# Optimization experiments

Hardware: AMD Instinct MI355X
Metric: run time of the kernel (lower is better)

## Reference

```python
import jax, jax.numpy as jnp
import numpy as np

B, H, N, D = 4, 16, 2048, 64


def setup_inputs() -> dict:
    key = jax.random.key(0)
    kq, kk, kv, km, kb = jax.random.split(key, 5)
    q = jax.random.normal(kq, (B, H, N, D), dtype=jnp.float32)
    k = jax.random.normal(kk, (B, H, N, D), dtype=jnp.float32)
    v = jax.random.normal(kv, (B, H, N, D), dtype=jnp.float32)
    # mostly-True mask so no row is fully masked
    mask = jax.random.uniform(km, (B, 1, N, N)) > 0.1
    attn_bias = jax.random.normal(kb, (1, H, N, N), dtype=jnp.float32)
    return {"q": q, "k": k, "v": v, "mask": mask, "attn_bias": attn_bias}


def reference(q, k, v, mask, attn_bias):
    scale = q.shape[-1] ** -0.5
    # sim: [B,H,N,N]
    sim = jnp.einsum('bhid,bhjd->bhij', q, k) * scale
    sim = sim + attn_bias
    neg = -jnp.finfo(sim.dtype).max
    sim = jnp.where(mask, sim, neg)
    attn = jax.nn.softmax(sim, axis=-1)
    out = jnp.einsum('bhij,bhjd->bhid', attn, v)
    return out
```

## Files before the change

### kernel.cpp

```cpp
#include <hip/hip_runtime.h>
#include <hip/hip_bf16.h>

typedef __bf16 bf16_t;
typedef bf16_t bf16x8 __attribute__((ext_vector_type(8)));
typedef float  floatx4 __attribute__((ext_vector_type(4)));

constexpr int Bb = 4, Hh = 16, Nn = 2048, Dd = 64;
constexpr int BM = 64;
constexpr int BN = 64;
constexpr int WM = 16;
constexpr float SCALE = 0.125f;
constexpr float NEG   = -3.4028234663852886e38f;

__global__ __launch_bounds__(256, 4)
void attn_fwd(const float* __restrict__ qg,
              const float* __restrict__ kg,
              const float* __restrict__ vg,
              const void*  __restrict__ maskg,
              const float* __restrict__ biasg,
              float* __restrict__ outg)
{
    __shared__ bf16x8 k_lds[512];
    __shared__ bf16x8 v_lds[512];
    __shared__ bf16x8 p_lds[4][128];

    const int tid  = threadIdx.x;
    const int wave = tid >> 6;
    const int lane = tid & 63;
    const int ln   = lane & 15;
    const int lq   = lane >> 4;

    const int id = blockIdx.x;
    const int b  = id & 3;
    const int h  = (id >> 2) & 15;
    const int mt = id >> 6;

    const int probe = ((const int*)maskg)[lane];
    const bool mask_i32 = __all(probe == 0 || probe == 1);
    const int*           mi = (const int*)maskg;
    const unsigned char* mb = (const unsigned char*)maskg;

    const size_t head  = (size_t)(b*Hh + h) * Nn * Dd;
    const int    qbase = mt*BM + wave*WM;

    bf16x8 qa[2];
    {
        const float* qp = qg + head + (size_t)(qbase + ln)*Dd + lq*8;
        #pragma unroll
        for (int kk = 0; kk < 2; ++kk) {
            float4 f0 = *(const float4*)(qp + kk*32);
            float4 f1 = *(const float4*)(qp + kk*32 + 4);
            bf16x8 a;
            a[0]=(bf16_t)f0.x; a[1]=(bf16_t)f0.y; a[2]=(bf16_t)f0.z; a[3]=(bf16_t)f0.w;
            a[4]=(bf16_t)f1.x; a[5]=(bf16_t)f1.y; a[6]=(bf16_t)f1.z; a[7]=(bf16_t)f1.w;
            qa[kk] = a;
        }
    }

    floatx4 o_acc[4];
    #pragma unroll
    for (int i = 0; i < 4; ++i) o_acc[i] = (floatx4){0.f,0.f,0.f,0.f};
    float mx[4], lsum[4];
    #pragma unroll
    for (int r = 0; r < 4; ++r) { mx[r] = -__builtin_inff(); lsum[r] = 0.f; }

    const int skey = tid >> 2;
    const int sd0  = (tid & 3) * 16;
    const int sblk = skey >> 4, sn = skey & 15;
    const int vkk  = skey >> 5, vq = (skey >> 3) & 3, vj = skey & 7;
    bf16_t* vl = (bf16_t*)v_lds;
    bf16_t* pl = (bf16_t*)p_lds[wave];

    for (int kt = 0; kt < Nn/BN; ++kt) {
        __syncthreads();
        {
            const float* kp = kg + head + (size_t)(kt*BN + skey)*Dd + sd0;
            const float* vp = vg + head + (size_t)(kt*BN + skey)*Dd + sd0;
            float kvv[16], vvv[16];
            *(float4*)(kvv+ 0) = *(const float4*)(kp+ 0);
            *(float4*)(kvv+ 4) = *(const float4*)(kp+ 4);
            *(float4*)(kvv+ 8) = *(const float4*)(kp+ 8);
            *(float4*)(kvv+12) = *(const float4*)(kp+12);
            *(float4*)(vvv+ 0) = *(const float4*)(vp+ 0);
            *(float4*)(vvv+ 4) = *(const float4*)(vp+ 4);
            *(float4*)(vvv+ 8) = *(const float4*)(vp+ 8);
            *(float4*)(vvv+12) = *(const float4*)(vp+12);
            #pragma unroll
            for (int g = 0; g < 2; ++g) {
                const int dg = sd0 + g*8;
                const int kkg = dg >> 5, qg2 = (dg >> 3) & 3;
                bf16x8 c;
                #pragma unroll
                for (int j = 0; j < 8; ++j) c[j] = (bf16_t)kvv[g*8+j];
                k_lds[(sblk*2 + kkg)*64 + qg2*16 + sn] = c;
            }
            #pragma unroll
            for (int t = 0; t < 16; ++t) {
                const int d = sd0 + t;
                const int nb = d >> 4, nn2 = d & 15;
                vl[(((vkk*4 + nb)*64 + vq*16 + nn2) << 3) | vj] = (bf16_t)vvv[t];
            }
        }
        __syncthreads();

        floatx4 s_acc[4];
        #pragma unroll
        for (int i = 0; i < 4; ++i) s_acc[i] = (floatx4){0.f,0.f,0.f,0.f};
        #pragma unroll
        for (int blk = 0; blk < 4; ++blk)
            #pragma unroll
            for (int kk = 0; kk < 2; ++kk)
                s_acc[blk] = __builtin_amdgcn_mfma_f32_16x16x32_bf16(
                    qa[kk], k_lds[(blk*2+kk)*64 + lane], s_acc[blk], 0, 0, 0);

        float sv[4][4], rmax[4];
        const size_t col0 = (size_t)kt*BN + ln;
        #pragma unroll
        for (int r = 0; r < 4; ++r) {
            const int m = qbase + lq*4 + r;
            const size_t brow = ((size_t)h*Nn + m)*Nn + col0;
            const size_t mrow = ((size_t)b*Nn + m)*Nn + col0;
            rmax[r] = NEG;
            #pragma unroll
            for (int blk = 0; blk < 4; ++blk) {
                float val = s_acc[blk][r]*SCALE + biasg[brow + blk*16];
                const bool ok = mask_i32 ? (mi[mrow + blk*16] != 0)
                                         : (mb[mrow + blk*16] != 0);
                val = ok ? val : NEG;
                sv[r][blk] = val;
                rmax[r] = fmaxf(rmax[r], val);
            }
        }
        #pragma unroll
        for (int off = 1; off < 16; off <<= 1)
            #pragma unroll
            for (int r = 0; r < 4; ++r)
                rmax[r] = fmaxf(rmax[r], __shfl_xor(rmax[r], off, 64));

        float alph[4], rsum[4];
        bf16_t pb[4][4];
        #pragma unroll
        for (int r = 0; r < 4; ++r) {
            const float mnew = fmaxf(mx[r], rmax[r]);
            alph[r] = __expf(mx[r] - mnew);
            mx[r] = mnew;
            float s = 0.f;
            #pragma unroll
            for (int blk = 0; blk < 4; ++blk) {
                const bf16_t p = (bf16_t)__expf(sv[r][blk] - mnew);
                pb[r][blk] = p;
                s += (float)p;
            }
            rsum[r] = s;
        }
        #pragma unroll
        for (int off = 1; off < 16; off <<= 1)
            #pragma unroll
            for (int r = 0; r < 4; ++r)
                rsum[r] += __shfl_xor(rsum[r], off, 64);
        #pragma unroll
        for (int r = 0; r < 4; ++r) {
            lsum[r] = lsum[r]*alph[r] + rsum[r];
            #pragma unroll
            for (int nb = 0; nb < 4; ++nb)
                o_acc[nb][r] *= alph[r];
        }

        #pragma unroll
        for (int r = 0; r < 4; ++r) {
            const int m = lq*4 + r;
            #pragma unroll
            for (int blk = 0; blk < 4; ++blk) {
                const int key = blk*16 + ln;
                const int kk2 = key >> 5, q2 = (key >> 3) & 3, j2 = key & 7;
                pl[((kk2*64 + q2*16 + m) << 3) | j2] = pb[r][blk];
            }
        }
        __syncthreads();

        #pragma unroll
        for (int kk = 0; kk < 2; ++kk) {
            const bf16x8 pa = p_lds[wave][kk*64 + lane];
            #pragma unroll
            for (int nb = 0; nb < 4; ++nb)
                o_acc[nb] = __builtin_amdgcn_mfma_f32_16x16x32_bf16(
                    pa, v_lds[(kk*4+nb)*64 + lane], o_acc[nb], 0, 0, 0);
        }
    }

    #pragma unroll
    for (int r = 0; r < 4; ++r) {
        const int m = qbase + lq*4 + r;
        const float inv = 1.f / lsum[r];
        float* op = outg + head + (size_t)m*Dd + ln;
        #pragma unroll
        for (int nb = 0; nb < 4; ++nb)
            op[nb*16] = o_acc[nb][r] * inv;
    }
}

extern "C" void kernel_launch(void* const* d_in, const int* in_sizes, int n_in,
                              void* d_out, int out_size, void* d_ws, size_t ws_size,
                              hipStream_t stream) {
    const float* q    = (const float*)d_in[0];
    const float* k    = (const float*)d_in[1];
    const float* v    = (const float*)d_in[2];
    const void*  mask = d_in[3];
    const float* bias = (const float*)d_in[4];
    float* out = (float*)d_out;
    (void)in_sizes; (void)n_in; (void)out_size; (void)d_ws; (void)ws_size;

    const int grid = Bb * Hh * (Nn / BM);
    attn_fwd<<<grid, 256, 0, stream>>>(q, k, v, mask, bias, out);
}
```

Measured before the change: 1.011 ms.

## Pre-convert K and transpose V to bf16, drop LDS staging, swap MFMA operands

```diff
diff --git a/kernel.cpp b/kernel.cpp
--- a/kernel.cpp
+++ b/kernel.cpp
@@ -1,201 +1,232 @@
 #include <hip/hip_runtime.h>
 #include <hip/hip_bf16.h>
+#include <stdint.h>
 
 typedef __bf16 bf16_t;
 typedef bf16_t bf16x8 __attribute__((ext_vector_type(8)));
+typedef bf16_t bf16x4 __attribute__((ext_vector_type(4)));
 typedef float  floatx4 __attribute__((ext_vector_type(4)));
 
 constexpr int Bb = 4, Hh = 16, Nn = 2048, Dd = 64;
-constexpr int BM = 64;
-constexpr int BN = 64;
-constexpr int WM = 16;
 constexpr float SCALE = 0.125f;
-constexpr float NEG   = -3.4028234663852886e38f;
+constexpr float NEGF  = -3.4028234663852886e38f;
+constexpr size_t KELEMS = (size_t)Bb * Hh * Nn * Dd;
+
+__device__ __forceinline__ uint2 bperm64(uint2 v, int byteaddr) {
+    uint2 r;
+    r.x = (unsigned)__builtin_amdgcn_ds_bpermute(byteaddr, (int)v.x);
+    r.y = (unsigned)__builtin_amdgcn_ds_bpermute(byteaddr, (int)v.y);
+    return r;
+}
+
+__global__ __launch_bounds__(256)
+void cvt_k(const float* __restrict__ kg, bf16_t* __restrict__ kb) {
+    const size_t i = ((size_t)blockIdx.x * 256 + threadIdx.x) * 8;
+    float4 a = *(const float4*)(kg + i);
+    float4 b = *(const float4*)(kg + i + 4);
+    bf16x8 o;
+    o[0]=(bf16_t)a.x; o[1]=(bf16_t)a.y; o[2]=(bf16_t)a.z; o[3]=(bf16_t)a.w;
+    o[4]=(bf16_t)b.x; o[5]=(bf16_t)b.y; o[6]=(bf16_t)b.z; o[7]=(bf16_t)b.w;
+    *(bf16x8*)(kb + i) = o;
+}
+
+__global__ __launch_bounds__(256)
+void transpose_v(const float* __restrict__ vg, bf16_t* __restrict__ vt) {
+    __shared__ float tile[64][65];
+    const int id = blockIdx.x;
+    const int bh = id >> 5, kt = id & 31;
+    const int t  = threadIdx.x;
+    const float* src = vg + ((size_t)bh * Nn + kt * 64) * Dd;
+    {
+        const int key = t >> 2, d0 = (t & 3) * 16;
+        #pragma unroll
+        for (int i = 0; i < 4; ++i) {
+            float4 f = *(const float4*)(src + key * Dd + d0 + i * 4);
+            tile[key][d0 + i*4 + 0] = f.x; tile[key][d0 + i*4 + 1] = f.y;
+            tile[key][d0 + i*4 + 2] = f.z; tile[key][d0 + i*4 + 3] = f.w;
+        }
+    }
+    __syncthreads();
+    const int d = t >> 2, k0 = (t & 3) * 16;
+    bf16_t* dst = vt + ((size_t)bh * Dd + d) * Nn + kt * 64 + k0;
+    #pragma unroll
+    for (int g = 0; g < 2; ++g) {
+        bf16x8 o;
+        #pragma unroll
+        for (int i = 0; i < 8; ++i) o[i] = (bf16_t)tile[k0 + g*8 + i][d];
+        *(bf16x8*)(dst + g * 8) = o;
+    }
+}
 
 __global__ __launch_bounds__(256, 4)
 void attn_fwd(const float* __restrict__ qg,
-              const float* __restrict__ kg,
-              const float* __restrict__ vg,
+              const bf16_t* __restrict__ kb,
+              const bf16_t* __restrict__ vt,
               const void*  __restrict__ maskg,
               const float* __restrict__ biasg,
               float* __restrict__ outg)
 {
-    __shared__ bf16x8 k_lds[512];
-    __shared__ bf16x8 v_lds[512];
-    __shared__ bf16x8 p_lds[4][128];
-
     const int tid  = threadIdx.x;
     const int wave = tid >> 6;
     const int lane = tid & 63;
     const int ln   = lane & 15;
-    const int lq   = lane >> 4;
-
-    const int id = blockIdx.x;
-    const int b  = id & 3;
-    const int h  = (id >> 2) & 15;
-    const int mt = id >> 6;
+    const int q    = lane >> 4;
+
+    const int id  = blockIdx.x;
+    const int xcd = id & 7, s = id >> 3;
+    const int b   = s & 3;
+    const int hm  = xcd * 64 + (s >> 2);
+    const int h   = hm >> 5;
+    const int mt  = hm & 31;
 
     const int probe = ((const int*)maskg)[lane];
     const bool mask_i32 = __all(probe == 0 || probe == 1);
-    const int*           mi = (const int*)maskg;
-    const unsigned char* mb = (const unsigned char*)maskg;
-
-    const size_t head  = (size_t)(b*Hh + h) * Nn * Dd;
-    const int    qbase = mt*BM + wave*WM;
-
-    bf16x8 qa[2];
+
+    const size_t head  = (size_t)(b * Hh + h) * Nn * Dd;
+    const int    qbase = mt * 64 + wave * 16;
+    const int    m     = qbase + ln;
+
+    bf16x8 qf[2];
     {
-        const float* qp = qg + head + (size_t)(qbase + ln)*Dd + lq*8;
+        const float* qp = qg + head + (size_t)m * Dd + q * 8;
         #pragma unroll
         for (int kk = 0; kk < 2; ++kk) {
-            float4 f0 = *(const float4*)(qp + kk*32);
-            float4 f1 = *(const float4*)(qp + kk*32 + 4);
-            bf16x8 a;
-            a[0]=(bf16_t)f0.x; a[1]=(bf16_t)f0.y; a[2]=(bf16_t)f0.z; a[3]=(bf16_t)f0.w;
-            a[4]=(bf16_t)f1.x; a[5]=(bf16_t)f1.y; a[6]=(bf16_t)f1.z; a[7]=(bf16_t)f1.w;
-            qa[kk] = a;
+            float4 f0 = *(const float4*)(qp + kk * 32);
+            float4 f1 = *(const float4*)(qp + kk * 32 + 4);
+            bf16x8 t;
+            t[0]=(bf16_t)f0.x; t[1]=(bf16_t)f0.y; t[2]=(bf16_t)f0.z; t[3]=(bf16_t)f0.w;
+            t[4]=(bf16_t)f1.x; t[5]=(bf16_t)f1.y; t[6]=(bf16_t)f1.z; t[7]=(bf16_t)f1.w;
+            qf[kk] = t;
         }
     }
 
     floatx4 o_acc[4];
     #pragma unroll
-    for (int i = 0; i < 4; ++i) o_acc[i] = (floatx4){0.f,0.f,0.f,0.f};
-    float mx[4], lsum[4];
-    #pragma unroll
-    for (int r = 0; r < 4; ++r) { mx[r] = -__builtin_inff(); lsum[r] = 0.f; }
-
-    const int skey = tid >> 2;
-    const int sd0  = (tid & 3) * 16;
-    const int sblk = skey >> 4, sn = skey & 15;
-    const int vkk  = skey >> 5, vq = (skey >> 3) & 3, vj = skey & 7;
-    bf16_t* vl = (bf16_t*)v_lds;
-    bf16_t* pl = (bf16_t*)p_lds[wave];
-
-    for (int kt = 0; kt < Nn/BN; ++kt) {
-        __syncthreads();
-        {
-            const float* kp = kg + head + (size_t)(kt*BN + skey)*Dd + sd0;
-            const float* vp = vg + head + (size_t)(kt*BN + skey)*Dd + sd0;
-            float kvv[16], vvv[16];
-            *(float4*)(kvv+ 0) = *(const float4*)(kp+ 0);
-            *(float4*)(kvv+ 4) = *(const float4*)(kp+ 4);
-            *(float4*)(kvv+ 8) = *(const float4*)(kp+ 8);
-            *(float4*)(kvv+12) = *(const float4*)(kp+12);
-            *(float4*)(vvv+ 0) = *(const float4*)(vp+ 0);
-            *(float4*)(vvv+ 4) = *(const float4*)(vp+ 4);
-            *(float4*)(vvv+ 8) = *(const float4*)(vp+ 8);
-            *(float4*)(vvv+12) = *(const float4*)(vp+12);
-            #pragma unroll
-            for (int g = 0; g < 2; ++g) {
-                const int dg = sd0 + g*8;
-                const int kkg = dg >> 5, qg2 = (dg >> 3) & 3;
-                bf16x8 c;
-                #pragma unroll
-                for (int j = 0; j < 8; ++j) c[j] = (bf16_t)kvv[g*8+j];
-                k_lds[(sblk*2 + kkg)*64 + qg2*16 + sn] = c;
-            }
-            #pragma unroll
-            for (int t = 0; t < 16; ++t) {
-                const int d = sd0 + t;
-                const int nb = d >> 4, nn2 = d & 15;
-                vl[(((vkk*4 + nb)*64 + vq*16 + nn2) << 3) | vj] = (bf16_t)vvv[t];
-            }
-        }
-        __syncthreads();
-
-        floatx4 s_acc[4];
-        #pragma unroll
-        for (int i = 0; i < 4; ++i) s_acc[i] = (floatx4){0.f,0.f,0.f,0.f};
+    for (int i = 0; i < 4; ++i) o_acc[i] = (floatx4){0.f, 0.f, 0.f, 0.f};
+    float mx = -__builtin_inff(), lsum = 0.f;
+
+    const bf16_t* kptr = kb + head + (size_t)ln * Dd + q * 8;
+    const bf16_t* vptr = vt + head + (size_t)ln * Nn + q * 8;
+    const float*  bptr = biasg + ((size_t)h * Nn + m) * Nn + q * 4;
+    const int*           mip = (const int*)maskg + ((size_t)b * Nn + m) * Nn + q * 4;
+    const unsigned char* mbp = (const unsigned char*)maskg + ((size_t)b * Nn + m) * Nn + q * 4;
+
+    const int lo_src = (ln | ((lane & 16) << 1)) << 2;
+    const int hi_src = lo_src + (16 << 2);
+    const bool hiSel = (lane >= 32);
+
+    for (int kt = 0; kt < Nn / 64; ++kt) {
+        const int koff = kt * 64;
+
+        bf16x8 vf[2][4];
+        #pragma unroll
+        for (int kk = 0; kk < 2; ++kk)
+            #pragma unroll
+            for (int nb = 0; nb < 4; ++nb)
+                vf[kk][nb] = *(const bf16x8*)(vptr + (size_t)nb * 16 * Nn + koff + kk * 32);
+
+        floatx4 bias4[4];
         #pragma unroll
         for (int blk = 0; blk < 4; ++blk)
-            #pragma unroll
-            for (int kk = 0; kk < 2; ++kk)
-                s_acc[blk] = __builtin_amdgcn_mfma_f32_16x16x32_bf16(
-                    qa[kk], k_lds[(blk*2+kk)*64 + lane], s_acc[blk], 0, 0, 0);
-
-        float sv[4][4], rmax[4];
-        const size_t col0 = (size_t)kt*BN + ln;
-        #pragma unroll
-        for (int r = 0; r < 4; ++r) {
-            const int m = qbase + lq*4 + r;
-            const size_t brow = ((size_t)h*Nn + m)*Nn + col0;
-            const size_t mrow = ((size_t)b*Nn + m)*Nn + col0;
-            rmax[r] = NEG;
+            bias4[blk] = *(const floatx4*)(bptr + koff + blk * 16);
+
+        floatx4 madd[4];
+        if (mask_i32) {
             #pragma unroll
             for (int blk = 0; blk < 4; ++blk) {
-                float val = s_acc[blk][r]*SCALE + biasg[brow + blk*16];
-                const bool ok = mask_i32 ? (mi[mrow + blk*16] != 0)
-                                         : (mb[mrow + blk*16] != 0);
-                val = ok ? val : NEG;
-                sv[r][blk] = val;
-                rmax[r] = fmaxf(rmax[r], val);
-            }
-        }
-        #pragma unroll
-        for (int off = 1; off < 16; off <<= 1)
-            #pragma unroll
-            for (int r = 0; r < 4; ++r)
-                rmax[r] = fmaxf(rmax[r], __shfl_xor(rmax[r], off, 64));
-
-        float alph[4], rsum[4];
-        bf16_t pb[4][4];
-        #pragma unroll
-        for (int r = 0; r < 4; ++r) {
-            const float mnew = fmaxf(mx[r], rmax[r]);
-            alph[r] = __expf(mx[r] - mnew);
-            mx[r] = mnew;
-            float s = 0.f;
+                int4 t = *(const int4*)(mip + koff + blk * 16);
+                floatx4 f;
+                f[0] = t.x ? 0.f : NEGF; f[1] = t.y ? 0.f : NEGF;
+                f[2] = t.z ? 0.f : NEGF; f[3] = t.w ? 0.f : NEGF;
+                madd[blk] = f;
+            }
+        } else {
             #pragma unroll
             for (int blk = 0; blk < 4; ++blk) {
-                const bf16_t p = (bf16_t)__expf(sv[r][blk] - mnew);
-                pb[r][blk] = p;
-                s += (float)p;
-            }
-            rsum[r] = s;
-        }
-        #pragma unroll
-        for (int off = 1; off < 16; off <<= 1)
-            #pragma unroll
-            for (int r = 0; r < 4; ++r)
-                rsum[r] += __shfl_xor(rsum[r], off, 64);
-        #pragma unroll
-        for (int r = 0; r < 4; ++r) {
-            lsum[r] = lsum[r]*alph[r] + rsum[r];
-            #pragma unroll
-            for (int nb = 0; nb < 4; ++nb)
-                o_acc[nb][r] *= alph[r];
-        }
-
-        #pragma unroll
-        for (int r = 0; r < 4; ++r) {
-            const int m = lq*4 + r;
-            #pragma unroll
-            for (int blk = 0; blk < 4; ++blk) {
-                const int key = blk*16 + ln;
-                const int kk2 = key >> 5, q2 = (key >> 3) & 3, j2 = key & 7;
-                pl[((kk2*64 + q2*16 + m) << 3) | j2] = pb[r][blk];
-            }
-        }
-        __syncthreads();
+                uint32_t t = *(const uint32_t*)(mbp + koff + blk * 16);
+                floatx4 f;
+                f[0] = (t & 0xffu)       ? 0.f : NEGF;
+                f[1] = (t & 0xff00u)     ? 0.f : NEGF;
+                f[2] = (t & 0xff0000u)   ? 0.f : NEGF;
+                f[3] = (t & 0xff000000u) ? 0.f : NEGF;
+                madd[blk] = f;
+            }
+        }
+
+        floatx4 sacc[4];
+        #pragma unroll
+        for (int blk = 0; blk < 4; ++blk) {
+            const bf16_t* kr = kptr + (size_t)(koff + blk * 16) * Dd;
+            bf16x8 ka = *(const bf16x8*)(kr);
+            bf16x8 kc = *(const bf16x8*)(kr + 32);
+            floatx4 acc = (floatx4){0.f, 0.f, 0.f, 0.f};
+            acc = __builtin_amdgcn_mfma_f32_16x16x32_bf16(ka, qf[0], acc, 0, 0, 0);
+            acc = __builtin_amdgcn_mfma_f32_16x16x32_bf16(kc, qf[1], acc, 0, 0, 0);
+            sacc[blk] = acc;
+        }
+
+        float sv[16];
+        float rmax = NEGF;
+        #pragma unroll
+        for (int blk = 0; blk < 4; ++blk)
+            #pragma unroll
+            for (int r = 0; r < 4; ++r) {
+                float val = fmaf(sacc[blk][r], SCALE, bias4[blk][r]) + madd[blk][r];
+                sv[blk * 4 + r] = val;
+                rmax = fmaxf(rmax, val);
+            }
+        rmax = fmaxf(rmax, __shfl_xor(rmax, 16, 64));
+        rmax = fmaxf(rmax, __shfl_xor(rmax, 32, 64));
+
+        const float mnew  = fmaxf(mx, rmax);
+        const float alpha = __expf(mx - mnew);
+        mx = mnew;
+
+        float rsum = 0.f;
+        uint2 pb[4];
+        #pragma unroll
+        for (int blk = 0; blk < 4; ++blk) {
+            bf16x4 p4;
+            #pragma unroll
+            for (int r = 0; r < 4; ++r) {
+                const bf16_t p = (bf16_t)__expf(sv[blk * 4 + r] - mnew);
+                p4[r] = p;
+                rsum += (float)p;
+            }
+            pb[blk] = __builtin_bit_cast(uint2, p4);
+        }
+        rsum += __shfl_xor(rsum, 16, 64);
+        rsum += __shfl_xor(rsum, 32, 64);
+        lsum = lsum * alpha + rsum;
+        #pragma unroll
+        for (int nb = 0; nb < 4; ++nb)
+            o_acc[nb] *= alpha;
 
         #pragma unroll
         for (int kk = 0; kk < 2; ++kk) {
-            const bf16x8 pa = p_lds[wave][kk*64 + lane];
+            uint2 a0 = bperm64(pb[2 * kk],     lo_src);
+            uint2 b0 = bperm64(pb[2 * kk + 1], lo_src);
+            uint2 a1 = bperm64(pb[2 * kk],     hi_src);
+            uint2 b1 = bperm64(pb[2 * kk + 1], hi_src);
+            uint2 lo = hiSel ? b0 : a0;
+            uint2 hi = hiSel ? b1 : a1;
+            uint4 pw = make_uint4(lo.x, lo.y, hi.x, hi.y);
+            bf16x8 pf = __builtin_bit_cast(bf16x8, pw);
             #pragma unroll
             for (int nb = 0; nb < 4; ++nb)
                 o_acc[nb] = __builtin_amdgcn_mfma_f32_16x16x32_bf16(
-                    pa, v_lds[(kk*4+nb)*64 + lane], o_acc[nb], 0, 0, 0);
-        }
-    }
-
+                    vf[kk][nb], pf, o_acc[nb], 0, 0, 0);
+        }
+    }
+
+    const float inv = 1.f / lsum;
+    float* op = outg + head + (size_t)m * Dd + q * 4;
     #pragma unroll
-    for (int r = 0; r < 4; ++r) {
-        const int m = qbase + lq*4 + r;
-        const float inv = 1.f / lsum[r];
-        float* op = outg + head + (size_t)m*Dd + ln;
-        #pragma unroll
-        for (int nb = 0; nb < 4; ++nb)
-            op[nb*16] = o_acc[nb][r] * inv;
+    for (int nb = 0; nb < 4; ++nb) {
+        float4 o;
+        o.x = o_acc[nb][0] * inv; o.y = o_acc[nb][1] * inv;
+        o.z = o_acc[nb][2] * inv; o.w = o_acc[nb][3] * inv;
+        *(float4*)(op + nb * 16) = o;
     }
 }
 
@@ -208,8 +239,12 @@
     const void*  mask = d_in[3];
     const float* bias = (const float*)d_in[4];
     float* out = (float*)d_out;
-    (void)in_sizes; (void)n_in; (void)out_size; (void)d_ws; (void)ws_size;
-
-    const int grid = Bb * Hh * (Nn / BM);
-    attn_fwd<<<grid, 256, 0, stream>>>(q, k, v, mask, bias, out);
-}
+    (void)in_sizes; (void)n_in; (void)out_size; (void)ws_size;
+
+    bf16_t* kbf = (bf16_t*)d_ws;
+    bf16_t* vtb = kbf + KELEMS;
+
+    cvt_k<<<(int)(KELEMS / (256 * 8)), 256, 0, stream>>>(k, kbf);
+    transpose_v<<<Bb * Hh * (Nn / 64), 256, 0, stream>>>(v, vtb);
+    attn_fwd<<<Bb * Hh * (Nn / 64), 256, 0, stream>>>(q, kbf, vtb, mask, bias, out);
+}
```

Result: slower. 1.064 ms (+5.2%).
